# Kernel tuning notes

Hardware: AMD Instinct MI355X
Metric: run time of the kernel (lower is better)

## Reference

```python
import jax, jax.numpy as jnp
import numpy as np


def _graph_conv(x, W, b, src, dst, norm_src, norm_dst, n_nodes):
    # DGL GraphConv, norm='both': out = D_in^{-1/2} * A * D_out^{-1/2} * x * W + b
    h = x * norm_src[:, None]                      # [N, d] scale by src out-degree norm
    m = h[src]                                     # [E, d] gather (irregular access)
    agg = jax.ops.segment_sum(m, dst, num_segments=n_nodes)  # [N, d] scatter-add
    agg = agg * norm_dst[:, None]
    return agg @ W + b


def setup_inputs() -> dict:
    key = jax.random.key(0)
    ks = jax.random.split(key, 6)
    N, E, IN, HID = 50000, 800000, 64, 128
    in_feat = jax.random.normal(ks[0], (N, IN), dtype=jnp.float32)
    W1 = jax.random.normal(ks[1], (IN, HID), dtype=jnp.float32) * (1.0 / np.sqrt(IN))
    b1 = jnp.zeros((HID,), dtype=jnp.float32)
    W2 = jax.random.normal(ks[2], (HID, IN), dtype=jnp.float32) * (1.0 / np.sqrt(HID))
    b2 = jnp.zeros((IN,), dtype=jnp.float32)
    src = jax.random.randint(ks[3], (E,), 0, N, dtype=jnp.int32)
    dst = jax.random.randint(ks[4], (E,), 0, N, dtype=jnp.int32)
    return {"in_feat": in_feat, "W1": W1, "b1": b1, "W2": W2, "b2": b2,
            "src": src, "dst": dst, "n_nodes": N}


def reference(in_feat, W1, b1, W2, b2, src, dst, n_nodes):
    ones = jnp.ones(src.shape, dtype=in_feat.dtype)
    deg_out = jax.ops.segment_sum(ones, src, num_segments=n_nodes)
    deg_in = jax.ops.segment_sum(ones, dst, num_segments=n_nodes)
    # DGL clamps degrees to min 1 (allow_zero_in_degree=True just skips the check)
    norm_src = jnp.clip(deg_out, 1.0, None) ** -0.5
    norm_dst = jnp.clip(deg_in, 1.0, None) ** -0.5
    h = _graph_conv(in_feat, W1, b1, src, dst, norm_src, norm_dst, n_nodes)
    h = jax.nn.relu(h)
    h = _graph_conv(h, W2, b2, src, dst, norm_src, norm_dst, n_nodes)
    return h
```

## Files before the change

### kernel.cpp

```cpp
#include <hip/hip_runtime.h>

#define IN_F 64
#define HID_F 128
#define CAP 64
#define CHUNK 8192
#define CAPB 4096
#define MAXB 512
#define CAPB32 1024
#define MAXB32 2048

typedef unsigned short u16;
typedef unsigned int u32;
typedef _Float16 f16;
typedef __attribute__((ext_vector_type(4))) _Float16 f16x4;
typedef __attribute__((ext_vector_type(8))) _Float16 f16x8;
typedef __attribute__((ext_vector_type(8))) u16 u16x8;
typedef __attribute__((ext_vector_type(4))) float f32x4;

__global__ __launch_bounds__(256)
void partition_kernel(const int* __restrict__ src, const int* __restrict__ dst,
                      int* __restrict__ gcurD, int* __restrict__ gcurS,
                      u32* __restrict__ bufD, u16* __restrict__ bufS,
                      const float* __restrict__ W1, const float* __restrict__ W2,
                      f16* __restrict__ W1t, f16* __restrict__ W2t,
                      f16* __restrict__ scaled_x, f16* __restrict__ g2,
                      int E, int NB32, int NBS, int N) {
    if (blockIdx.x == gridDim.x - 1) {
        for (int t = threadIdx.x; t < 2 * IN_F * HID_F; t += 256) {
            if (t < IN_F * HID_F) {
                int n = t / IN_F, k = t % IN_F;
                W1t[t] = (f16)W1[k * HID_F + n];
            } else {
                int i = t - IN_F * HID_F;
                int n = i / HID_F, k = i % HID_F;
                W2t[i] = (f16)W2[k * IN_F + n];
            }
        }
        for (int t = threadIdx.x; t < IN_F; t += 256) {
            scaled_x[(size_t)N * IN_F + t] = (f16)0.f;
            g2[(size_t)N * IN_F + t]       = (f16)0.f;
        }
        return;
    }
    __shared__ int histD[MAXB32], baseD[MAXB32], histS[MAXB], baseS[MAXB];
    const int t  = threadIdx.x;
    const int e0 = blockIdx.x * CHUNK;
    const int n  = min(CHUNK, E - e0);

    int ed[32], es[32];

    for (int b = t; b < NB32; b += 256) histD[b] = 0;
    for (int b = t; b < NBS;  b += 256) histS[b] = 0;
    __syncthreads();
#pragma unroll
    for (int j = 0; j < 32; ++j) {
        int i = t + j * 256;
        if (i < n) {
            ed[j] = dst[e0 + i];
            es[j] = src[e0 + i];
            atomicAdd(&histD[ed[j] >> 5], 1);
            atomicAdd(&histS[es[j] >> 7], 1);
        }
    }
    __syncthreads();
    for (int b = t; b < NB32; b += 256) {
        baseD[b] = atomicAdd(&gcurD[b], histD[b]);
        histD[b] = 0;
    }
    for (int b = t; b < NBS; b += 256) {
        baseS[b] = atomicAdd(&gcurS[b], histS[b]);
        histS[b] = 0;
    }
    __syncthreads();
#pragma unroll
    for (int j = 0; j < 32; ++j) {
        int i = t + j * 256;
        if (i < n) {
            int d  = ed[j];
            int s  = es[j];
            int bD = d >> 5, bS = s >> 7;
            int p  = baseD[bD] + atomicAdd(&histD[bD], 1);
            if (p < CAPB32)
                bufD[(size_t)bD * CAPB32 + p] = (u32)s | ((u32)(d & 31) << 16);
            int p2 = baseS[bS] + atomicAdd(&histS[bS], 1);
            if (p2 < CAPB) bufS[(size_t)bS * CAPB + p2] = (u16)s;
        }
    }
}

__global__ __launch_bounds__(256)
void srcprep_kernel(const u16* __restrict__ bufS, const int* __restrict__ gcurS,
                    float* __restrict__ norm_src,
                    const float* __restrict__ x, f16x4* __restrict__ scaled_x,
                    int N) {
    __shared__ int lcur[128];
    const int t = threadIdx.x;
    if (t < 128) lcur[t] = 0;
    __syncthreads();
    const int b = blockIdx.x;
    const int cnt = min(gcurS[b], CAPB);
    const u16* p = bufS + (size_t)b * CAPB;
    for (int i = t; i < cnt; i += 256)
        atomicAdd(&lcur[p[i] & 127], 1);
    __syncthreads();
    const int node0 = b * 128;
    if (t < 128 && node0 + t < N)
        norm_src[node0 + t] = rsqrtf((float)max(lcur[t], 1));
    for (int i = t; i < 128 * 16; i += 256) {
        int r = i >> 4, c = i & 15;
        int node = node0 + r;
        if (node < N) {
            float ns = rsqrtf((float)max(lcur[r], 1));
            float4 v = ((const float4*)x)[(size_t)node * 16 + c];
            f16x4 h;
            h.x = (f16)(v.x * ns); h.y = (f16)(v.y * ns);
            h.z = (f16)(v.z * ns); h.w = (f16)(v.w * ns);
            scaled_x[(size_t)node * 16 + c] = h;
        }
    }
}

__global__ __launch_bounds__(256)
void gather_gemm_kernel(const u32* __restrict__ bufD, const int* __restrict__ gcurD,
                        const f16x8* __restrict__ xs,
                        const f16* __restrict__ W1t, const float* __restrict__ b1,
                        const float* __restrict__ ns,
                        const f16* __restrict__ W2t, f16* __restrict__ g2,
                        u16* __restrict__ slots_g, int* __restrict__ deg_g, int N) {
    constexpr int LDX = IN_F + 8;
    constexpr int LDH = HID_F + 8;
    __shared__ __align__(16) u16 sl[32 * CAP];
    __shared__ int lcur[32];
    __shared__ float snd[32];
    __shared__ __align__(16) f16 sx[32 * LDX];
    __shared__ __align__(16) f16 h[2][16 * LDH];

    const int t  = threadIdx.x;
    const int b  = blockIdx.x;
    const int r0 = b * 32;

    {
        u16x8 sv;
#pragma unroll
        for (int k = 0; k < 8; ++k) sv[k] = (u16)N;
        ((u16x8*)sl)[t] = sv;
    }
    if (t < 32) lcur[t] = 0;
    __syncthreads();
    const int cnt = min(gcurD[b], CAPB32);
    const u32* p = bufD + (size_t)b * CAPB32;
    for (int i = t; i < cnt; i += 256) {
        u32 v = p[i];
        int din = (int)(v >> 16);
        int pos = atomicAdd(&lcur[din], 1);
        if (pos < CAP) sl[din * CAP + pos] = (u16)(v & 0xFFFFu);
    }
    __syncthreads();
    if (t < 32) {
        snd[t] = rsqrtf((float)max(lcur[t], 1));
        if (r0 + t < N) deg_g[r0 + t] = lcur[t];
    }
    __syncthreads();

    ((u16x8*)slots_g)[(size_t)b * 256 + t] = ((const u16x8*)sl)[t];

    const int row = t >> 3;
    const int c   = t & 7;
    float acc[8];
#pragma unroll
    for (int k = 0; k < 8; ++k) acc[k] = 0.f;
    {
        int degR = (min(lcur[row], CAP) + 15) & ~15;
        for (int i = 0; i < degR; i += 16) {
            u16x8 sa = *(const u16x8*)(sl + row * CAP + i);
            u16x8 sb = *(const u16x8*)(sl + row * CAP + i + 8);
            f16x8 v[16];
#pragma unroll
            for (int j = 0; j < 8; ++j) v[j]     = xs[(size_t)sa[j] * 8 + c];
#pragma unroll
            for (int j = 0; j < 8; ++j) v[8 + j] = xs[(size_t)sb[j] * 8 + c];
#pragma unroll
            for (int j = 0; j < 16; ++j)
#pragma unroll
                for (int k = 0; k < 8; ++k) acc[k] += (float)v[j][k];
        }
    }
    {
        f16x8 hv;
#pragma unroll
        for (int k = 0; k < 8; ++k) hv[k] = (f16)acc[k];
        *(f16x8*)&sx[row * LDX + c * 8] = hv;
    }
    __syncthreads();

    const int wave = t >> 6;
    const int lane = t & 63;
    const int nl   = lane & 15;
    const int quad = lane >> 4;

#pragma unroll
    for (int rt = 0; rt < 2; ++rt) {
        f16x8 a1[2];
#pragma unroll
        for (int kf = 0; kf < 2; ++kf)
            a1[kf] = *(const f16x8*)(sx + (rt * 16 + nl) * LDX + kf * 32 + quad * 8);

        float rs1[4];
#pragma unroll
        for (int reg = 0; reg < 4; ++reg)
            rs1[reg] = snd[rt * 16 + quad * 4 + reg];

        f16* hb = h[rt];
#pragma unroll
        for (int cti = 0; cti < 2; ++cti) {
            const int ct = wave * 2 + cti;
            f32x4 acc1 = (f32x4){0.f, 0.f, 0.f, 0.f};
#pragma unroll
            for (int kf = 0; kf < 2; ++kf) {
                f16x8 bf = *(const f16x8*)(W1t + (ct * 16 + nl) * IN_F + kf * 32 + quad * 8);
                acc1 = __builtin_amdgcn_mfma_f32_16x16x32_f16(a1[kf], bf, acc1, 0, 0, 0);
            }
            float bb = b1[ct * 16 + nl];
#pragma unroll
            for (int reg = 0; reg < 4; ++reg) {
                float v = fmaxf(acc1[reg] * rs1[reg] + bb, 0.f);
                hb[(quad * 4 + reg) * LDH + ct * 16 + nl] = (f16)v;
            }
        }
    }
    __syncthreads();

#pragma unroll
    for (int rt = 0; rt < 2; ++rt) {
        f32x4 acc2 = (f32x4){0.f, 0.f, 0.f, 0.f};
#pragma unroll
        for (int kf = 0; kf < 4; ++kf) {
            f16x8 a2 = *(const f16x8*)(h[rt] + nl * LDH + kf * 32 + quad * 8);
            f16x8 bf = *(const f16x8*)(W2t + (wave * 16 + nl) * HID_F + kf * 32 + quad * 8);
            acc2 = __builtin_amdgcn_mfma_f32_16x16x32_f16(a2, bf, acc2, 0, 0, 0);
        }

        float rs2[4];
#pragma unroll
        for (int reg = 0; reg < 4; ++reg)
            rs2[reg] = ns[min(r0 + rt * 16 + quad * 4 + reg, N - 1)];
#pragma unroll
        for (int reg = 0; reg < 4; ++reg) {
            int r = r0 + rt * 16 + quad * 4 + reg;
            if (r < N)
                g2[(size_t)r * IN_F + wave * 16 + nl] = (f16)(acc2[reg] * rs2[reg]);
        }
    }
}

__global__ __launch_bounds__(256)
void gather_out_kernel(const f16x8* __restrict__ xs, const u16* __restrict__ slots_g,
                       const int* __restrict__ deg_g, const float* __restrict__ bias,
                       float4* __restrict__ out, int N) {
    int tg = blockIdx.x * blockDim.x + threadIdx.x;
    int node = tg >> 3;
    int c = tg & 7;
    if (node >= N) return;
    int deg  = deg_g[node];
    int degR = (min(deg, CAP) + 15) & ~15;
    const u16* srow = slots_g + (size_t)node * CAP;
    float acc[8];
#pragma unroll
    for (int k = 0; k < 8; ++k) acc[k] = 0.f;

    for (int i = 0; i < degR; i += 16) {
        u16x8 sa = *(const u16x8*)(srow + i);
        u16x8 sb = *(const u16x8*)(srow + i + 8);
        f16x8 v[16];
#pragma unroll
        for (int j = 0; j < 8; ++j) v[j]     = xs[(size_t)sa[j] * 8 + c];
#pragma unroll
        for (int j = 0; j < 8; ++j) v[8 + j] = xs[(size_t)sb[j] * 8 + c];
#pragma unroll
        for (int j = 0; j < 16; ++j)
#pragma unroll
            for (int k = 0; k < 8; ++k) acc[k] += (float)v[j][k];
    }
    float d = rsqrtf((float)max(deg, 1));
    float4 b0 = ((const float4*)bias)[c * 2];
    float4 b1v = ((const float4*)bias)[c * 2 + 1];
    float4 o0, o1;
    o0.x = acc[0] * d + b0.x;  o0.y = acc[1] * d + b0.y;
    o0.z = acc[2] * d + b0.z;  o0.w = acc[3] * d + b0.w;
    o1.x = acc[4] * d + b1v.x; o1.y = acc[5] * d + b1v.y;
    o1.z = acc[6] * d + b1v.z; o1.w = acc[7] * d + b1v.w;
    out[(size_t)node * 16 + c * 2]     = o0;
    out[(size_t)node * 16 + c * 2 + 1] = o1;
}

extern "C" void kernel_launch(void* const* d_in, const int* in_sizes, int n_in,
                              void* d_out, int out_size, void* d_ws, size_t ws_size,
                              hipStream_t stream) {
    const float* in_feat = (const float*)d_in[0];
    const float* W1      = (const float*)d_in[1];
    const float* b1      = (const float*)d_in[2];
    const float* W2      = (const float*)d_in[3];
    const float* b2      = (const float*)d_in[4];
    const int*   src     = (const int*)d_in[5];
    const int*   dst     = (const int*)d_in[6];

    const int N = in_sizes[0] / IN_F;
    const int E = in_sizes[5];
    float* out = (float*)d_out;

    const int NB32 = (N + 31) >> 5;
    const int NBS  = (N + 127) >> 7;

    int* gcurD      = (int*)d_ws;
    int* gcurS      = gcurD + MAXB32;
    int* deg_g      = gcurS + MAXB;
    float* norm_src = (float*)(deg_g + N);
    f16* scaled_x   = (f16*)(norm_src + N);
    f16* g2         = scaled_x + (size_t)(N + 1) * IN_F;
    f16* W1t        = g2 + (size_t)(N + 1) * IN_F;
    f16* W2t        = W1t + IN_F * HID_F;
    u32* bufD       = (u32*)(W2t + IN_F * HID_F);
    u16* slots_g    = (u16*)(bufD + (size_t)MAXB32 * CAPB32);
    u16* bufS       = slots_g + (size_t)N * CAP;

    hipMemsetAsync(gcurD, 0, sizeof(int) * (MAXB32 + MAXB), stream);
    partition_kernel<<<(E + CHUNK - 1) / CHUNK + 1, 256, 0, stream>>>(
        src, dst, gcurD, gcurS, bufD, bufS, W1, W2, W1t, W2t,
        scaled_x, g2, E, NB32, NBS, N);

    srcprep_kernel<<<NBS, 256, 0, stream>>>(
        bufS, gcurS, norm_src, in_feat, (f16x4*)scaled_x, N);

    gather_gemm_kernel<<<NB32, 256, 0, stream>>>(
        bufD, gcurD, (const f16x8*)scaled_x, W1t, b1, norm_src, W2t, g2,
        slots_g, deg_g, N);

    gather_out_kernel<<<(N * 8 + 255) / 256, 256, 0, stream>>>(
        (const f16x8*)g2, slots_g, deg_g, b2, (float4*)out, N);
}
```

Measured before the change: 150.3 us.

## Count source out-degrees with global atomics instead of bucketed source partition

```diff
diff --git a/kernel.cpp b/kernel.cpp
--- a/kernel.cpp
+++ b/kernel.cpp
@@ -3,9 +3,7 @@
 #define IN_F 64
 #define HID_F 128
 #define CAP 64
-#define CHUNK 8192
-#define CAPB 4096
-#define MAXB 512
+#define CHUNK 2048
 #define CAPB32 1024
 #define MAXB32 2048
 
@@ -19,12 +17,12 @@
 
 __global__ __launch_bounds__(256)
 void partition_kernel(const int* __restrict__ src, const int* __restrict__ dst,
-                      int* __restrict__ gcurD, int* __restrict__ gcurS,
-                      u32* __restrict__ bufD, u16* __restrict__ bufS,
+                      int* __restrict__ gcurD, int* __restrict__ deg_out,
+                      u32* __restrict__ bufD,
                       const float* __restrict__ W1, const float* __restrict__ W2,
                       f16* __restrict__ W1t, f16* __restrict__ W2t,
                       f16* __restrict__ scaled_x, f16* __restrict__ g2,
-                      int E, int NB32, int NBS, int N) {
+                      int E, int NB32, int N) {
     if (blockIdx.x == gridDim.x - 1) {
         for (int t = threadIdx.x; t < 2 * IN_F * HID_F; t += 256) {
             if (t < IN_F * HID_F) {
@@ -42,82 +40,63 @@
         }
         return;
     }
-    __shared__ int histD[MAXB32], baseD[MAXB32], histS[MAXB], baseS[MAXB];
+    __shared__ int histD[MAXB32], baseD[MAXB32];
     const int t  = threadIdx.x;
     const int e0 = blockIdx.x * CHUNK;
     const int n  = min(CHUNK, E - e0);
 
-    int ed[32], es[32];
+    int ed[8];
 
     for (int b = t; b < NB32; b += 256) histD[b] = 0;
-    for (int b = t; b < NBS;  b += 256) histS[b] = 0;
-    __syncthreads();
-#pragma unroll
-    for (int j = 0; j < 32; ++j) {
+    __syncthreads();
+#pragma unroll
+    for (int j = 0; j < 8; ++j) {
         int i = t + j * 256;
         if (i < n) {
             ed[j] = dst[e0 + i];
-            es[j] = src[e0 + i];
             atomicAdd(&histD[ed[j] >> 5], 1);
-            atomicAdd(&histS[es[j] >> 7], 1);
+            atomicAdd(&deg_out[src[e0 + i]], 1);
         }
     }
     __syncthreads();
     for (int b = t; b < NB32; b += 256) {
-        baseD[b] = atomicAdd(&gcurD[b], histD[b]);
+        int h = histD[b];
+        if (h) baseD[b] = atomicAdd(&gcurD[b], h);
         histD[b] = 0;
     }
-    for (int b = t; b < NBS; b += 256) {
-        baseS[b] = atomicAdd(&gcurS[b], histS[b]);
-        histS[b] = 0;
-    }
-    __syncthreads();
-#pragma unroll
-    for (int j = 0; j < 32; ++j) {
+    __syncthreads();
+#pragma unroll
+    for (int j = 0; j < 8; ++j) {
         int i = t + j * 256;
         if (i < n) {
             int d  = ed[j];
-            int s  = es[j];
-            int bD = d >> 5, bS = s >> 7;
+            int s  = src[e0 + i];
+            int bD = d >> 5;
             int p  = baseD[bD] + atomicAdd(&histD[bD], 1);
             if (p < CAPB32)
                 bufD[(size_t)bD * CAPB32 + p] = (u32)s | ((u32)(d & 31) << 16);
-            int p2 = baseS[bS] + atomicAdd(&histS[bS], 1);
-            if (p2 < CAPB) bufS[(size_t)bS * CAPB + p2] = (u16)s;
         }
     }
 }
 
 __global__ __launch_bounds__(256)
-void srcprep_kernel(const u16* __restrict__ bufS, const int* __restrict__ gcurS,
-                    float* __restrict__ norm_src,
-                    const float* __restrict__ x, f16x4* __restrict__ scaled_x,
+void srcprep_kernel(const int* __restrict__ deg_out, float* __restrict__ norm_src,
+                    const float* __restrict__ x, f16x8* __restrict__ scaled_x,
                     int N) {
-    __shared__ int lcur[128];
-    const int t = threadIdx.x;
-    if (t < 128) lcur[t] = 0;
-    __syncthreads();
-    const int b = blockIdx.x;
-    const int cnt = min(gcurS[b], CAPB);
-    const u16* p = bufS + (size_t)b * CAPB;
-    for (int i = t; i < cnt; i += 256)
-        atomicAdd(&lcur[p[i] & 127], 1);
-    __syncthreads();
-    const int node0 = b * 128;
-    if (t < 128 && node0 + t < N)
-        norm_src[node0 + t] = rsqrtf((float)max(lcur[t], 1));
-    for (int i = t; i < 128 * 16; i += 256) {
-        int r = i >> 4, c = i & 15;
-        int node = node0 + r;
-        if (node < N) {
-            float ns = rsqrtf((float)max(lcur[r], 1));
-            float4 v = ((const float4*)x)[(size_t)node * 16 + c];
-            f16x4 h;
-            h.x = (f16)(v.x * ns); h.y = (f16)(v.y * ns);
-            h.z = (f16)(v.z * ns); h.w = (f16)(v.w * ns);
-            scaled_x[(size_t)node * 16 + c] = h;
-        }
-    }
+    const int tg = blockIdx.x * 256 + threadIdx.x;
+    const int node = tg >> 3;
+    const int c = tg & 7;
+    if (node >= N) return;
+    float nsv = rsqrtf((float)max(deg_out[node], 1));
+    if (c == 0) norm_src[node] = nsv;
+    float4 a = ((const float4*)x)[(size_t)node * 16 + c * 2];
+    float4 b = ((const float4*)x)[(size_t)node * 16 + c * 2 + 1];
+    f16x8 h;
+    h[0] = (f16)(a.x * nsv); h[1] = (f16)(a.y * nsv);
+    h[2] = (f16)(a.z * nsv); h[3] = (f16)(a.w * nsv);
+    h[4] = (f16)(b.x * nsv); h[5] = (f16)(b.y * nsv);
+    h[6] = (f16)(b.z * nsv); h[7] = (f16)(b.w * nsv);
+    scaled_x[(size_t)node * 8 + c] = h;
 }
 
 __global__ __launch_bounds__(256)
@@ -309,11 +288,10 @@
     float* out = (float*)d_out;
 
     const int NB32 = (N + 31) >> 5;
-    const int NBS  = (N + 127) >> 7;
 
     int* gcurD      = (int*)d_ws;
-    int* gcurS      = gcurD + MAXB32;
-    int* deg_g      = gcurS + MAXB;
+    int* deg_out    = gcurD + MAXB32;
+    int* deg_g      = deg_out + N;
     float* norm_src = (float*)(deg_g + N);
     f16* scaled_x   = (f16*)(norm_src + N);
     f16* g2         = scaled_x + (size_t)(N + 1) * IN_F;
@@ -321,15 +299,14 @@
     f16* W2t        = W1t + IN_F * HID_F;
     u32* bufD       = (u32*)(W2t + IN_F * HID_F);
     u16* slots_g    = (u16*)(bufD + (size_t)MAXB32 * CAPB32);
-    u16* bufS       = slots_g + (size_t)N * CAP;
-
-    hipMemsetAsync(gcurD, 0, sizeof(int) * (MAXB32 + MAXB), stream);
+
+    hipMemsetAsync(gcurD, 0, sizeof(int) * (MAXB32 + N), stream);
     partition_kernel<<<(E + CHUNK - 1) / CHUNK + 1, 256, 0, stream>>>(
-        src, dst, gcurD, gcurS, bufD, bufS, W1, W2, W1t, W2t,
-        scaled_x, g2, E, NB32, NBS, N);
-
-    srcprep_kernel<<<NBS, 256, 0, stream>>>(
-        bufS, gcurS, norm_src, in_feat, (f16x4*)scaled_x, N);
+        src, dst, gcurD, deg_out, bufD, W1, W2, W1t, W2t,
+        scaled_x, g2, E, NB32, N);
+
+    srcprep_kernel<<<(N * 8 + 255) / 256, 256, 0, stream>>>(
+        deg_out, norm_src, in_feat, (f16x8*)scaled_x, N);
 
     gather_gemm_kernel<<<NB32, 256, 0, stream>>>(
         bufD, gcurD, (const f16x8*)scaled_x, W1t, b1, norm_src, W2t, g2,
```

New measurement: 176.5 us. 17.5% more time.
